# Kernel optimization log

Measured on AMD Instinct MI355X. Metric: run time of the kernel, lower is better.

The kernel has to match this reference:

```python
import jax, jax.numpy as jnp
import numpy as np

N = 8192
IN_DIM = 512
OUT_DIM = 256
ALPHA = 0.2  # LeakyReLU negative slope


def setup_inputs() -> dict:
    key = jax.random.key(0)
    k_nodes, k_edge, k_W, k_Wb, k_a1, k_a1b, k_a2, k_a2b = jax.random.split(key, 8)
    nodes = jax.random.normal(k_nodes, (N, IN_DIM), dtype=jnp.float32)
    edge_mat = jax.random.uniform(k_edge, (N, N)) > 0.5
    edge_mat = edge_mat | jnp.eye(N, dtype=bool)
    s_W = 1.0 / np.sqrt(IN_DIM)
    s_a = 1.0 / np.sqrt(OUT_DIM)
    W_w = jax.random.uniform(k_W, (OUT_DIM, IN_DIM), minval=-s_W, maxval=s_W, dtype=jnp.float32)
    W_b = jax.random.uniform(k_Wb, (OUT_DIM,), minval=-s_W, maxval=s_W, dtype=jnp.float32)
    a1_w = jax.random.uniform(k_a1, (1, OUT_DIM), minval=-s_a, maxval=s_a, dtype=jnp.float32)
    a1_b = jax.random.uniform(k_a1b, (1,), minval=-s_a, maxval=s_a, dtype=jnp.float32)
    a2_w = jax.random.uniform(k_a2, (1, OUT_DIM), minval=-s_a, maxval=s_a, dtype=jnp.float32)
    a2_b = jax.random.uniform(k_a2b, (1,), minval=-s_a, maxval=s_a, dtype=jnp.float32)
    return {"nodes": nodes, "edge_mat": edge_mat, "W_w": W_w, "W_b": W_b,
            "a1_w": a1_w, "a1_b": a1_b, "a2_w": a2_w, "a2_b": a2_b}


def reference(nodes, edge_mat, W_w, W_b, a1_w, a1_b, a2_w, a2_b):
    Wh = nodes @ W_w.T + W_b                      # [N, OUT_DIM]
    Wh1 = Wh @ a1_w.T + a1_b                      # [N, 1]
    Wh2 = Wh @ a2_w.T + a2_b                      # [N, 1]
    scores = jax.nn.leaky_relu(Wh1 + Wh2.T, negative_slope=ALPHA)  # [N, N]
    masked = jnp.where(edge_mat, scores, -jnp.inf)
    attention = jax.nn.softmax(masked, axis=1)    # [N, N]
    return attention @ Wh                         # [N, OUT_DIM]
```

## Files before the change

### kernel.cpp

```cpp
#include <hip/hip_runtime.h>
#include <hip/hip_bf16.h>
#include <stdint.h>


#define NN 8192
#define IND 512
#define OUTD 256

typedef __attribute__((ext_vector_type(8))) short short8;
typedef __attribute__((ext_vector_type(4))) short short4v;
typedef __attribute__((ext_vector_type(4))) float f32x4;
typedef __attribute__((ext_vector_type(4))) unsigned int u32x4;

#define AS_GLOBAL __attribute__((address_space(1)))
#define AS_LDS __attribute__((address_space(3)))

static __device__ __forceinline__ short f2bf(float f) {
  return __builtin_bit_cast(short, __float2bfloat16(f));
}

extern "C" __global__ __launch_bounds__(256) void k_convert_w(
    const float* __restrict__ W, short* __restrict__ W2) {
  const int t = blockIdx.x * 256 + threadIdx.x;
  const int row = t >> 6, kb = t & 63;
  const float* src = W + row * IND + kb * 8;
  f32x4 x0 = *(const f32x4*)src;
  f32x4 x1 = *(const f32x4*)(src + 4);
  short8 o;
  o[0] = f2bf(x0[0]); o[1] = f2bf(x0[1]); o[2] = f2bf(x0[2]); o[3] = f2bf(x0[3]);
  o[4] = f2bf(x1[0]); o[5] = f2bf(x1[1]); o[6] = f2bf(x1[2]); o[7] = f2bf(x1[3]);
  *(short8*)(W2 + (size_t)kb * 2048 + row * 8) = o;
}

extern "C" __global__ __launch_bounds__(256, 2) void k_front(
    const int* __restrict__ mask, uint32_t* __restrict__ bm,
    const float* __restrict__ nodes, const short* __restrict__ W2,
    const float* __restrict__ Wb, const float* __restrict__ a1w,
    const float* __restrict__ a1b, const float* __restrict__ a2w,
    const float* __restrict__ a2b, short* __restrict__ WhL,
    float* __restrict__ sAC, uint32_t* __restrict__ sPK) {
  const int bid = blockIdx.x;
  const int tid = threadIdx.x;
  const int wv = tid >> 6, lane = tid & 63;

  if (bid % 9 != 8) {
    const int mb = (bid / 9) * 8 + (bid % 9);
    const int gw = mb * 4 + wv;
    const size_t base = (size_t)gw * 16384;
#pragma unroll 4
    for (int it = 0; it < 64; ++it) {
      const size_t ib = base + (size_t)it * 256;
      unsigned long long b0 = __ballot(mask[ib + lane] != 0);
      unsigned long long b1 = __ballot(mask[ib + 64 + lane] != 0);
      unsigned long long b2 = __ballot(mask[ib + 128 + lane] != 0);
      unsigned long long b3 = __ballot(mask[ib + 192 + lane] != 0);
      if (lane < 8) {
        unsigned long long s01 = (lane & 2) ? b1 : b0;
        unsigned long long s23 = (lane & 2) ? b3 : b2;
        unsigned long long sel = (lane & 4) ? s23 : s01;
        bm[ib / 32 + lane] = (uint32_t)(sel >> ((lane & 1) * 32));
      }
    }
    return;
  }

  const int wb = bid / 9;
  const int g = lane >> 4, m = lane & 15;
  const int rowbase = wb * 64 + wv * 16;

  f32x4 acc[16];
#pragma unroll
  for (int nf = 0; nf < 16; ++nf) acc[nf] = (f32x4){0.f, 0.f, 0.f, 0.f};

  const float* arow = nodes + (size_t)(rowbase + m) * IND;
  const short* bb = W2 + (size_t)g * 2048 + m * 8;
#pragma unroll 4
  for (int k0 = 0; k0 < IND; k0 += 32) {
    const float* ap = arow + k0 + g * 8;
    f32x4 x0 = *(const f32x4*)ap;
    f32x4 x1 = *(const f32x4*)(ap + 4);
    short8 af;
    af[0] = f2bf(x0[0]); af[1] = f2bf(x0[1]); af[2] = f2bf(x0[2]); af[3] = f2bf(x0[3]);
    af[4] = f2bf(x1[0]); af[5] = f2bf(x1[1]); af[6] = f2bf(x1[2]); af[7] = f2bf(x1[3]);
    const short* bk = bb + (size_t)(k0 >> 3) * 2048;
#pragma unroll
    for (int nf = 0; nf < 16; ++nf) {
      short8 bf = *(const short8*)(bk + nf * 128);
      acc[nf] = __builtin_amdgcn_mfma_f32_16x16x32_bf16(af, bf, acc[nf], 0, 0, 0);
    }
  }

  float p1[4] = {0.f, 0.f, 0.f, 0.f}, p2[4] = {0.f, 0.f, 0.f, 0.f};
#pragma unroll
  for (int nf = 0; nf < 16; ++nf) {
    const int n = nf * 16 + m;
    const float b = Wb[n], c1 = a1w[n], c2 = a2w[n];
#pragma unroll
    for (int r = 0; r < 4; ++r) {
      float v = acc[nf][r] + b;
      acc[nf][r] = v;
      p1[r] += c1 * v;
      p2[r] += c2 * v;
    }
  }
#pragma unroll
  for (int off = 1; off < 16; off <<= 1) {
#pragma unroll
    for (int r = 0; r < 4; ++r) {
      p1[r] += __shfl_xor(p1[r], off);
      p2[r] += __shfl_xor(p2[r], off);
    }
  }
  if (m == 0) {
    const float b1 = a1b[0], b2 = a2b[0];
#pragma unroll
    for (int r = 0; r < 4; ++r) {
      const int row = rowbase + g * 4 + r;
      const float v1 = p1[r] + b1, v2 = p2[r] + b2;
      sAC[row] = __expf(v1);
      sAC[NN + row] = __expf(0.2f * v1);
      const float B = __expf(v2), D = __expf(0.2f * v2);
      sPK[row] = ((uint32_t)(uint16_t)f2bf(B) << 16) | (uint16_t)f2bf(D);
    }
  }

  const size_t cbase = ((size_t)(rowbase >> 3) + (g >> 1)) * 2048 + (g & 1) * 4;
#pragma unroll
  for (int nf = 0; nf < 16; ++nf) {
    short4v o;
#pragma unroll
    for (int r = 0; r < 4; ++r) o[r] = f2bf(acc[nf][r]);
    *(short4v*)(WhL + cbase + (size_t)(nf * 16 + m) * 8) = o;
  }
}

extern "C" __global__ __launch_bounds__(512, 4) void k_attn(
    const uint32_t* __restrict__ bm, const short* __restrict__ WhL,
    const float* __restrict__ sAC, const uint32_t* __restrict__ sPK,
    float* __restrict__ pnum, float* __restrict__ pden) {
  __shared__ char smem[69632];
  uint32_t* PKs = (uint32_t*)(smem + 49152);
  uint32_t* BMs = (uint32_t*)(smem + 53248);

  const int tid = threadIdx.x;
  const int w = tid >> 6, lane = tid & 63, g = lane >> 4, m = lane & 15;
  const int rt = blockIdx.x >> 3, jc = blockIdx.x & 7;
  const int rg = w & 3, ns = w >> 2;
  const int rb = rt * 128 + rg * 32;

  const float A0 = sAC[rb + m],      A1 = sAC[rb + 16 + m];
  const float C0 = sAC[NN + rb + m], C1 = sAC[NN + rb + 16 + m];

  f32x4 acc0[8], acc1[8];
#pragma unroll
  for (int nf = 0; nf < 8; ++nf) {
    acc0[nf] = (f32x4){0.f, 0.f, 0.f, 0.f};
    acc1[nf] = (f32x4){0.f, 0.f, 0.f, 0.f};
  }
  float den0 = 0.f, den1 = 0.f;

  {
    const int rloc = tid >> 2, wq = (tid & 3) * 8;
    const uint32_t* src = bm + (size_t)(rt * 128 + rloc) * 256 + jc * 32 + wq;
    u32x4 a = *(const u32x4*)src;
    u32x4 b = *(const u32x4*)(src + 4);
#pragma unroll
    for (int i = 0; i < 4; ++i)
      BMs[rloc * 32 + ((wq + i) ^ (rloc & 31))] = a[i];
#pragma unroll
    for (int i = 0; i < 4; ++i)
      BMs[rloc * 32 + ((wq + 4 + i) ^ (rloc & 31))] = b[i];
  }
  if (tid < 256) {
    __builtin_amdgcn_global_load_lds(
        (const AS_GLOBAL void*)((const char*)sPK + (size_t)jc * 4096 + tid * 16),
        (AS_LDS void*)(smem + 49152 + tid * 16), 16, 0, 0);
  }
  const short* gS = WhL + (size_t)jc * 262144;
#pragma unroll
  for (int s = 0; s < 2; ++s) {
#pragma unroll
    for (int c = 0; c < 2; ++c) {
      __builtin_amdgcn_global_load_lds(
          (const AS_GLOBAL void*)(gS + s * 8192 + w * 1024 + c * 512 + lane * 8),
          (AS_LDS void*)(smem + s * 16384 + w * 2048 + c * 1024), 16, 0, 0);
    }
  }
  __syncthreads();

  auto build = [&](float A, float C, uint32_t mbits,
                   const u32x4& q0, const u32x4& q1, float& den) -> short8 {
    short8 af;
#pragma unroll
    for (int i = 0; i < 8; ++i) {
      const uint32_t pw = (i < 4) ? q0[i] : q1[i - 4];
      const float D = __builtin_bit_cast(float, pw << 16);
      const float B = __builtin_bit_cast(float, pw & 0xFFFF0000u);
      const float val = fmaxf(A * B, C * D);
      const float pv = ((mbits >> i) & 1u) ? val : 0.f;
      den += pv;
      af[i] = f2bf(pv);
    }
    return af;
  };

  for (int u = 0; u < 32; ++u) {
    asm volatile("s_waitcnt vmcnt(2)" ::: "memory");
    __builtin_amdgcn_s_barrier();
    __builtin_amdgcn_sched_barrier(0);

    {
      const int up = (u + 2 < 32) ? (u + 2) : 31;
      const int bi = (u + 2) % 3;
      const short* gn = gS + up * 8192 + w * 1024 + lane * 8;
      char* ldb = smem + bi * 16384 + w * 2048;
      __builtin_amdgcn_global_load_lds((const AS_GLOBAL void*)gn,
                                       (AS_LDS void*)ldb, 16, 0, 0);
      __builtin_amdgcn_global_load_lds((const AS_GLOBAL void*)(gn + 512),
                                       (AS_LDS void*)(ldb + 1024), 16, 0, 0);
    }

    const uint32_t cw0 = BMs[(rg * 32 + m) * 32 + (u ^ m)];
    const uint32_t cw1 = BMs[(rg * 32 + 16 + m) * 32 + (u ^ (16 + m))];
    const uint32_t* pk = &PKs[u * 32 + g * 8];
    const u32x4 q0 = *(const u32x4*)(pk + 0);
    const u32x4 q1 = *(const u32x4*)(pk + 4);
    short8 af0 = build(A0, C0, cw0 >> (g * 8), q0, q1, den0);
    short8 af1 = build(A1, C1, cw1 >> (g * 8), q0, q1, den1);

    const short* bl = (const short*)(smem + (u % 3) * 16384) +
                      g * 2048 + (ns * 128 + m) * 8;
#pragma unroll
    for (int nf = 0; nf < 8; ++nf) {
      short8 bf = *(const short8*)(bl + nf * 128);
      acc0[nf] = __builtin_amdgcn_mfma_f32_16x16x32_bf16(af0, bf, acc0[nf], 0, 0, 0);
      acc1[nf] = __builtin_amdgcn_mfma_f32_16x16x32_bf16(af1, bf, acc1[nf], 0, 0, 0);
    }
  }

  den0 += __shfl_xor(den0, 16); den0 += __shfl_xor(den0, 32);
  den1 += __shfl_xor(den1, 16); den1 += __shfl_xor(den1, 32);
  if (ns == 0 && lane < 16) {
    pden[jc * NN + rb + m] = den0;
    pden[jc * NN + rb + 16 + m] = den1;
  }

  float* pn = pnum + (size_t)jc * NN * OUTD + (size_t)rb * OUTD + ns * 128;
#pragma unroll
  for (int r = 0; r < 4; ++r) {
    const int q = g * 4 + r;
#pragma unroll
    for (int nf = 0; nf < 8; ++nf) {
      pn[(size_t)q * OUTD + nf * 16 + m] = acc0[nf][r];
      pn[(size_t)(16 + q) * OUTD + nf * 16 + m] = acc1[nf][r];
    }
  }
}

extern "C" __global__ __launch_bounds__(256) void k_comb(
    const float* __restrict__ pnum, const float* __restrict__ pden,
    float* __restrict__ out) {
  const int idx = blockIdx.x * 256 + threadIdx.x;
  const int row = idx >> 6, c4 = (idx & 63) * 4;
  f32x4 s = (f32x4){0.f, 0.f, 0.f, 0.f};
  float d = 0.f;
#pragma unroll
  for (int jc = 0; jc < 8; ++jc) {
    f32x4 v = *(const f32x4*)(pnum + ((size_t)jc * NN + row) * OUTD + c4);
    s += v;
    d += pden[jc * NN + row];
  }
  const float inv = 1.f / d;
  *(f32x4*)(out + (size_t)row * OUTD + c4) = s * inv;
}

extern "C" void kernel_launch(void* const* d_in, const int* in_sizes, int n_in,
                              void* d_out, int out_size, void* d_ws, size_t ws_size,
                              hipStream_t stream) {
  const float* nodes = (const float*)d_in[0];
  const int*   mask  = (const int*)d_in[1];
  const float* W_w   = (const float*)d_in[2];
  const float* W_b   = (const float*)d_in[3];
  const float* a1w   = (const float*)d_in[4];
  const float* a1b   = (const float*)d_in[5];
  const float* a2w   = (const float*)d_in[6];
  const float* a2b   = (const float*)d_in[7];
  float* out = (float*)d_out;

  char* ws = (char*)d_ws;
  short*    WhL  = (short*)(ws);
  short*    W2   = (short*)(ws + (size_t)4  * 1024 * 1024 + 65536);
  uint32_t* bmp  = (uint32_t*)(ws + (size_t)5  * 1024 * 1024);
  float*    sAC  = (float*)(ws + (size_t)13 * 1024 * 1024);
  uint32_t* sPK  = (uint32_t*)(ws + (size_t)14 * 1024 * 1024);
  float*    pnum = (float*)(ws + (size_t)16 * 1024 * 1024);
  float*    pden = (float*)(ws + (size_t)96 * 1024 * 1024);

  hipLaunchKernelGGL(k_convert_w, dim3(64), dim3(256), 0, stream, W_w, W2);
  hipLaunchKernelGGL(k_front, dim3(1152), dim3(256), 0, stream,
                     mask, bmp, nodes, W2, W_b, a1w, a1b, a2w, a2b,
                     WhL, sAC, sPK);
  hipLaunchKernelGGL(k_attn, dim3(512), dim3(512), 0, stream,
                     bmp, WhL, sAC, sPK, pnum, pden);
  hipLaunchKernelGGL(k_comb, dim3(2048), dim3(256), 0, stream,
                     pnum, pden, out);
}
```

Baseline: 169.7 us.

## Replace LDS-staged attention loop with direct register double-buffered global loads

The attention kernel stops staging WhL, packed scores and mask bits in shared memory behind block barriers. Each wave now loads its own B fragments, packed coefficients and mask words straight into registers, double-buffered two iterations ahead. The row tile shrinks from 128 to 64 rows, the grid doubles to 1024 blocks, and MFMA issue is wrapped in a raised s_setprio. This removes barriers and LDS traffic but gives up sharing of loaded data within the block, so global/L2 load traffic rises and register pressure may grow.

```diff
diff --git a/kernel.cpp b/kernel.cpp
--- a/kernel.cpp
+++ b/kernel.cpp
@@ -138,55 +138,47 @@
     const uint32_t* __restrict__ bm, const short* __restrict__ WhL,
     const float* __restrict__ sAC, const uint32_t* __restrict__ sPK,
     float* __restrict__ pnum, float* __restrict__ pden) {
-  __shared__ char smem[69632];
-  uint32_t* PKs = (uint32_t*)(smem + 49152);
-  uint32_t* BMs = (uint32_t*)(smem + 53248);
-
   const int tid = threadIdx.x;
   const int w = tid >> 6, lane = tid & 63, g = lane >> 4, m = lane & 15;
   const int rt = blockIdx.x >> 3, jc = blockIdx.x & 7;
-  const int rg = w & 3, ns = w >> 2;
-  const int rb = rt * 128 + rg * 32;
+  const int rg = w & 1, ns = w >> 1;
+  const int rb = rt * 64 + rg * 32;
 
   const float A0 = sAC[rb + m],      A1 = sAC[rb + 16 + m];
   const float C0 = sAC[NN + rb + m], C1 = sAC[NN + rb + 16 + m];
 
-  f32x4 acc0[8], acc1[8];
-#pragma unroll
-  for (int nf = 0; nf < 8; ++nf) {
+  f32x4 acc0[4], acc1[4];
+#pragma unroll
+  for (int nf = 0; nf < 4; ++nf) {
     acc0[nf] = (f32x4){0.f, 0.f, 0.f, 0.f};
     acc1[nf] = (f32x4){0.f, 0.f, 0.f, 0.f};
   }
   float den0 = 0.f, den1 = 0.f;
 
-  {
-    const int rloc = tid >> 2, wq = (tid & 3) * 8;
-    const uint32_t* src = bm + (size_t)(rt * 128 + rloc) * 256 + jc * 32 + wq;
-    u32x4 a = *(const u32x4*)src;
-    u32x4 b = *(const u32x4*)(src + 4);
-#pragma unroll
-    for (int i = 0; i < 4; ++i)
-      BMs[rloc * 32 + ((wq + i) ^ (rloc & 31))] = a[i];
-#pragma unroll
-    for (int i = 0; i < 4; ++i)
-      BMs[rloc * 32 + ((wq + 4 + i) ^ (rloc & 31))] = b[i];
-  }
-  if (tid < 256) {
-    __builtin_amdgcn_global_load_lds(
-        (const AS_GLOBAL void*)((const char*)sPK + (size_t)jc * 4096 + tid * 16),
-        (AS_LDS void*)(smem + 49152 + tid * 16), 16, 0, 0);
-  }
-  const short* gS = WhL + (size_t)jc * 262144;
-#pragma unroll
-  for (int s = 0; s < 2; ++s) {
-#pragma unroll
-    for (int c = 0; c < 2; ++c) {
-      __builtin_amdgcn_global_load_lds(
-          (const AS_GLOBAL void*)(gS + s * 8192 + w * 1024 + c * 512 + lane * 8),
-          (AS_LDS void*)(smem + s * 16384 + w * 2048 + c * 1024), 16, 0, 0);
-    }
-  }
-  __syncthreads();
+  const uint32_t* bw0 = bm + (size_t)(rb + m) * 256 + jc * 32;
+  const uint32_t* bw1 = bw0 + (size_t)16 * 256;
+  const short* gB = WhL + (size_t)jc * 262144 + (size_t)g * 2048 +
+                    (ns * 64 + m) * 8;
+  const uint32_t* gP = sPK + (size_t)jc * 1024 + g * 8;
+
+  struct Win {
+    short8 b0, b1, b2, b3;
+    u32x4 q0, q1;
+    uint32_t c0, c1;
+  };
+
+  auto issue = [&](int v, Win& W_) {
+    const short* p = gB + (size_t)v * 8192;
+    W_.b0 = *(const short8*)(p);
+    W_.b1 = *(const short8*)(p + 128);
+    W_.b2 = *(const short8*)(p + 256);
+    W_.b3 = *(const short8*)(p + 384);
+    const uint32_t* pp = gP + v * 32;
+    W_.q0 = *(const u32x4*)(pp);
+    W_.q1 = *(const u32x4*)(pp + 4);
+    W_.c0 = bw0[v];
+    W_.c1 = bw1[v];
+  };
 
   auto build = [&](float A, float C, uint32_t mbits,
                    const u32x4& q0, const u32x4& q1, float& den) -> short8 {
@@ -204,38 +196,33 @@
     return af;
   };
 
-  for (int u = 0; u < 32; ++u) {
-    asm volatile("s_waitcnt vmcnt(2)" ::: "memory");
-    __builtin_amdgcn_s_barrier();
+  auto compute = [&](const Win& W_) {
+    short8 af0 = build(A0, C0, W_.c0 >> (g * 8), W_.q0, W_.q1, den0);
+    short8 af1 = build(A1, C1, W_.c1 >> (g * 8), W_.q0, W_.q1, den1);
+    __builtin_amdgcn_s_setprio(1);
+    acc0[0] = __builtin_amdgcn_mfma_f32_16x16x32_bf16(af0, W_.b0, acc0[0], 0, 0, 0);
+    acc1[0] = __builtin_amdgcn_mfma_f32_16x16x32_bf16(af1, W_.b0, acc1[0], 0, 0, 0);
+    acc0[1] = __builtin_amdgcn_mfma_f32_16x16x32_bf16(af0, W_.b1, acc0[1], 0, 0, 0);
+    acc1[1] = __builtin_amdgcn_mfma_f32_16x16x32_bf16(af1, W_.b1, acc1[1], 0, 0, 0);
+    acc0[2] = __builtin_amdgcn_mfma_f32_16x16x32_bf16(af0, W_.b2, acc0[2], 0, 0, 0);
+    acc1[2] = __builtin_amdgcn_mfma_f32_16x16x32_bf16(af1, W_.b2, acc1[2], 0, 0, 0);
+    acc0[3] = __builtin_amdgcn_mfma_f32_16x16x32_bf16(af0, W_.b3, acc0[3], 0, 0, 0);
+    acc1[3] = __builtin_amdgcn_mfma_f32_16x16x32_bf16(af1, W_.b3, acc1[3], 0, 0, 0);
+    __builtin_amdgcn_s_setprio(0);
+  };
+
+  Win WA, WB;
+  issue(0, WA);
+  issue(1, WB);
+  for (int u = 0; u < 32; u += 2) {
+    asm volatile("s_waitcnt vmcnt(8)" ::: "memory");
     __builtin_amdgcn_sched_barrier(0);
-
-    {
-      const int up = (u + 2 < 32) ? (u + 2) : 31;
-      const int bi = (u + 2) % 3;
-      const short* gn = gS + up * 8192 + w * 1024 + lane * 8;
-      char* ldb = smem + bi * 16384 + w * 2048;
-      __builtin_amdgcn_global_load_lds((const AS_GLOBAL void*)gn,
-                                       (AS_LDS void*)ldb, 16, 0, 0);
-      __builtin_amdgcn_global_load_lds((const AS_GLOBAL void*)(gn + 512),
-                                       (AS_LDS void*)(ldb + 1024), 16, 0, 0);
-    }
-
-    const uint32_t cw0 = BMs[(rg * 32 + m) * 32 + (u ^ m)];
-    const uint32_t cw1 = BMs[(rg * 32 + 16 + m) * 32 + (u ^ (16 + m))];
-    const uint32_t* pk = &PKs[u * 32 + g * 8];
-    const u32x4 q0 = *(const u32x4*)(pk + 0);
-    const u32x4 q1 = *(const u32x4*)(pk + 4);
-    short8 af0 = build(A0, C0, cw0 >> (g * 8), q0, q1, den0);
-    short8 af1 = build(A1, C1, cw1 >> (g * 8), q0, q1, den1);
-
-    const short* bl = (const short*)(smem + (u % 3) * 16384) +
-                      g * 2048 + (ns * 128 + m) * 8;
-#pragma unroll
-    for (int nf = 0; nf < 8; ++nf) {
-      short8 bf = *(const short8*)(bl + nf * 128);
-      acc0[nf] = __builtin_amdgcn_mfma_f32_16x16x32_bf16(af0, bf, acc0[nf], 0, 0, 0);
-      acc1[nf] = __builtin_amdgcn_mfma_f32_16x16x32_bf16(af1, bf, acc1[nf], 0, 0, 0);
-    }
+    compute(WA);
+    issue((u + 2 < 32) ? u + 2 : 31, WA);
+    asm volatile("s_waitcnt vmcnt(8)" ::: "memory");
+    __builtin_amdgcn_sched_barrier(0);
+    compute(WB);
+    issue((u + 3 < 32) ? u + 3 : 31, WB);
   }
 
   den0 += __shfl_xor(den0, 16); den0 += __shfl_xor(den0, 32);
@@ -245,12 +232,12 @@
     pden[jc * NN + rb + 16 + m] = den1;
   }
 
-  float* pn = pnum + (size_t)jc * NN * OUTD + (size_t)rb * OUTD + ns * 128;
+  float* pn = pnum + (size_t)jc * NN * OUTD + (size_t)rb * OUTD + ns * 64;
 #pragma unroll
   for (int r = 0; r < 4; ++r) {
     const int q = g * 4 + r;
 #pragma unroll
-    for (int nf = 0; nf < 8; ++nf) {
+    for (int nf = 0; nf < 4; ++nf) {
       pn[(size_t)q * OUTD + nf * 16 + m] = acc0[nf][r];
       pn[(size_t)(16 + q) * OUTD + nf * 16 + m] = acc1[nf][r];
     }
@@ -300,7 +287,7 @@
   hipLaunchKernelGGL(k_front, dim3(1152), dim3(256), 0, stream,
                      mask, bmp, nodes, W2, W_b, a1w, a1b, a2w, a2b,
                      WhL, sAC, sPK);
-  hipLaunchKernelGGL(k_attn, dim3(512), dim3(512), 0, stream,
+  hipLaunchKernelGGL(k_attn, dim3(1024), dim3(512), 0, stream,
                      bmp, WhL, sAC, sPK, pnum, pden);
   hipLaunchKernelGGL(k_comb, dim3(2048), dim3(256), 0, stream,
                      pnum, pden, out);
```

After: 491.7 us. 2.9x slower.
